# Kernel tuning notes

Measured on AMD Instinct MI355X. Metric: run time of the kernel, lower is better.

Reference implementation:

```python
import jax, jax.numpy as jnp
import numpy as np

NBINS = (128, 64, 32)   # knots per stacked transform
N_GENES = 5000
N_ELEM = 4_000_000


def _split_parameters(unnormalized):
    # mirror of QuadraticSplineStack._split_parameters: [heights(n), widths(n-1)] per transform
    splits = []
    for n in NBINS:
        splits += [n, n - 1]
    parts = jnp.split(unnormalized, np.cumsum(splits)[:-1].tolist(), axis=-1)
    return list(zip(parts[0::2], parts[1::2]))


def _bin_search(table, gix, x):
    # vectorized per-element binary search: searchsorted(table[gix], x, side='right') - 1,
    # clamped to valid bin range [0, K-2]. table: [G, K] sorted; gix, x: [N].
    K = table.shape[-1]
    lo = jnp.zeros(x.shape, jnp.int32)
    hi = jnp.full(x.shape, K, jnp.int32)
    for _ in range(int(np.ceil(np.log2(K + 1)))):
        mid = jnp.clip((lo + hi) // 2, 0, K - 1)
        pred = table[gix, mid] <= x
        lo = jnp.where(pred, mid + 1, lo)
        hi = jnp.where(pred, hi, mid)
    return jnp.clip(lo - 1, 0, K - 2)


def _quadratic_spline_forward(x, gix, unnorm_heights, unnorm_widths):
    # per-gene tables
    widths = jax.nn.softmax(unnorm_widths, axis=-1)                      # [G, n-1]
    locs = jnp.cumsum(widths, axis=-1)
    locs = jnp.pad(locs.at[:, -1].set(1.0), ((0, 0), (1, 0)))            # [G, n] bin_locations
    eh = jnp.exp(unnorm_heights)                                         # [G, n]
    area = jnp.sum(0.5 * (eh[:, :-1] + eh[:, 1:]) * widths, axis=-1, keepdims=True)
    heights = eh / area                                                  # pdf knot heights, integrates to 1
    cdf = jnp.cumsum(0.5 * (heights[:, :-1] + heights[:, 1:]) * widths, axis=-1)
    left_cdf = jnp.pad(cdf.at[:, -1].set(1.0), ((0, 0), (1, 0)))         # [G, n] bin_left_cdf

    # locate bin per element, then gather scalar coefficients
    b = _bin_search(locs, gix, x)                                        # [N] in [0, n-2]
    w = widths[gix, b]
    lh = heights[gix, b]
    rh = heights[gix, b + 1]
    bl = locs[gix, b]
    lc = left_cdf[gix, b]

    alpha = (x - bl) / w
    out = (0.5 * (rh - lh) * w) * alpha * alpha + (lh * w) * alpha + lc
    out = jnp.clip(out, 0.0, 1.0)
    logabsdet = jnp.log(alpha * (rh - lh) + lh)
    return out, logabsdet


def setup_inputs() -> dict:
    key = jax.random.key(0)
    k1, k2, k3 = jax.random.split(key, 3)
    x = jax.random.uniform(k1, (N_ELEM,), dtype=jnp.float32, minval=1e-4, maxval=1.0 - 1e-4)
    local_gene_ix = jax.random.randint(k2, (N_ELEM,), 0, N_GENES)
    total = sum(n + (n - 1) for n in NBINS)  # 445
    unnormalized = jax.random.normal(k3, (N_GENES, total), dtype=jnp.float32) * 0.1
    return {"x": x, "local_gene_ix": local_gene_ix, "unnormalized": unnormalized}


def reference(x, local_gene_ix, unnormalized):
    gix = local_gene_ix.astype(jnp.int32)
    outputs = x
    logabsdet = jnp.zeros_like(x)
    for uh, uw in _split_parameters(unnormalized):
        outputs, lad = _quadratic_spline_forward(outputs, gix, uh, uw)
        logabsdet = logabsdet + lad
    return outputs, logabsdet
```

## Files before the change

### kernel.cpp

```cpp
#include <hip/hip_runtime.h>
#include <hip/hip_bf16.h>
#include <hip/hip_fp16.h>

#define N_GENES_MAX 5000
#define PARAMS_PER_GENE 445

#define KNOTS_PER_GENE 224

__device__ uint2 g_knots[(size_t)N_GENES_MAX * KNOTS_PER_GENE];

static __device__ __forceinline__ unsigned short f2h(float f) {
    union { __half h; unsigned short u; } c;
    c.h = __float2half_rn(f);
    return c.u;
}
static __device__ __forceinline__ float h2f(unsigned short u) {
    union { unsigned short u; __half h; } c;
    c.u = u;
    return __half2float(c.h);
}

__global__ void build_knots(const float* __restrict__ params) {
    const int g = blockIdx.x;
    const int t = blockIdx.y;
    const int ns[3]   = {128, 64, 32};
    const int poff[3] = {0, 255, 382};
    const int koff[3] = {0, 128, 192};

    const int n = ns[t];
    const int m = n - 1;
    const float* ph = params + (size_t)g * PARAMS_PER_GENE + poff[t];
    const float* pw = ph + n;

    __shared__ float s_scan[128];
    __shared__ float s_h[129];
    __shared__ float s_red[128];
    __shared__ float s_loc[128];
    __shared__ float s_cdf[128];

    const int tid = threadIdx.x;

    float uw = (tid < m) ? pw[tid] : -1e30f;
    s_red[tid] = uw;
    __syncthreads();
    for (int s = 64; s > 0; s >>= 1) {
        if (tid < s) s_red[tid] = fmaxf(s_red[tid], s_red[tid + s]);
        __syncthreads();
    }
    const float mx = s_red[0];
    __syncthreads();
    float e = (tid < m) ? expf(uw - mx) : 0.0f;

    s_scan[tid] = e;
    __syncthreads();
    #pragma unroll
    for (int off = 1; off < 128; off <<= 1) {
        float v = (tid >= off) ? s_scan[tid - off] : 0.0f;
        __syncthreads();
        s_scan[tid] += v;
        __syncthreads();
    }
    const float S = s_scan[m - 1];
    const float invS = 1.0f / S;
    const float w_i = e * invS;
    if (tid == 0) s_loc[0] = 0.0f;
    if (tid < m) s_loc[tid + 1] = (tid == m - 1) ? 1.0f : s_scan[tid] * invS;
    __syncthreads();

    float uh = (tid < n) ? ph[tid] : 0.0f;
    float eh = (tid < n) ? expf(uh) : 0.0f;
    s_h[tid] = eh;
    if (tid == 0) s_h[128] = 0.0f;
    __syncthreads();
    float term = (tid < m) ? 0.5f * (s_h[tid] + s_h[tid + 1]) * w_i : 0.0f;
    s_red[tid] = term;
    __syncthreads();
    for (int s = 64; s > 0; s >>= 1) {
        if (tid < s) s_red[tid] += s_red[tid + s];
        __syncthreads();
    }
    const float area = s_red[0];
    __syncthreads();
    const float inv_area = 1.0f / area;
    const float hgt = eh * inv_area;

    float d = term * inv_area;
    s_scan[tid] = d;
    __syncthreads();
    #pragma unroll
    for (int off = 1; off < 128; off <<= 1) {
        float v = (tid >= off) ? s_scan[tid - off] : 0.0f;
        __syncthreads();
        s_scan[tid] += v;
        __syncthreads();
    }
    if (tid == 0) s_cdf[0] = 0.0f;
    if (tid < m) s_cdf[tid + 1] = (tid == m - 1) ? 1.0f : s_scan[tid];
    __syncthreads();

    if (tid < n) {
        uint2 kt;
        kt.x = __float_as_uint(s_loc[tid]);
        kt.y = ((unsigned)f2h(s_cdf[tid]) << 16) | (unsigned)f2h(hgt);
        g_knots[(size_t)g * KNOTS_PER_GENE + koff[t] + tid] = kt;
    }
}

template <int K>
__device__ __forceinline__ void spline_stage(const uint2* __restrict__ kn,
                                             float& x, float& lad) {
    int b = (int)(x * (float)(K - 1));
    b = (b < 0) ? 0 : ((b > K - 2) ? K - 2 : b);
    uint2 k0 = kn[b];
    uint2 k1 = kn[b + 1];
    float l0 = __uint_as_float(k0.x);
    float l1 = __uint_as_float(k1.x);
    while (b > 0 && l0 > x) {
        --b;
        k1 = k0; l1 = l0;
        k0 = kn[b]; l0 = __uint_as_float(k0.x);
    }
    while (b < K - 2 && l1 <= x) {
        ++b;
        k0 = k1; l0 = l1;
        k1 = kn[b + 1]; l1 = __uint_as_float(k1.x);
    }
    const float lh = h2f((unsigned short)(k0.y & 0xffffu));
    const float lc = h2f((unsigned short)(k0.y >> 16));
    const float rh = h2f((unsigned short)(k1.y & 0xffffu));
    const float w  = l1 - l0;
    const float alpha = (x - l0) / w;
    float o = (0.5f * (rh - lh) * w) * alpha * alpha + (lh * w) * alpha + lc;
    o = fminf(fmaxf(o, 0.0f), 1.0f);
    lad += __logf(alpha * (rh - lh) + lh);
    x = o;
}

__global__ void spline_eval_gather(const float* __restrict__ x_in,
                                   const int* __restrict__ gix,
                                   float* __restrict__ out, int N) {
    const int i = blockIdx.x * blockDim.x + threadIdx.x;
    if (i >= N) return;
    float x = x_in[i];
    const uint2* tab = g_knots + (size_t)gix[i] * KNOTS_PER_GENE;
    float lad = 0.0f;
    spline_stage<128>(tab, x, lad);
    spline_stage<64>(tab + 128, x, lad);
    spline_stage<32>(tab + 192, x, lad);
    out[i] = x;
    out[N + i] = lad;
}

extern "C" void kernel_launch(void* const* d_in, const int* in_sizes, int n_in,
                              void* d_out, int out_size, void* d_ws, size_t ws_size,
                              hipStream_t stream) {
    const float* x      = (const float*)d_in[0];
    const int*   gix    = (const int*)d_in[1];
    const float* params = (const float*)d_in[2];
    float* out = (float*)d_out;

    const int N = in_sizes[0];
    const int G = in_sizes[2] / PARAMS_PER_GENE;

    build_knots<<<dim3(G, 3), 128, 0, stream>>>(params);

    const int block = 256;
    spline_eval_gather<<<(N + block - 1) / block, block, 0, stream>>>(x, gix, out, N);
}
```

Baseline: 212.2 us.

## Split knot tables per stage, use wave shuffles, process two elements per thread

The knot table is split into three separate per-stage arrays instead of one interleaved array per gene. The table-building kernel replaces its shared-memory tree reductions and scans with 64-lane wave shuffle primitives and fast exp. The stored CDF is now an fp16 offset relative to the knot location, which aims to reduce quantization error. The eval kernel handles two elements per thread using vectorized nontemporal loads and stores, which raises per-thread work and exposes more independent gathers at the cost of fewer threads.

```diff
diff --git a/kernel.cpp b/kernel.cpp
--- a/kernel.cpp
+++ b/kernel.cpp
@@ -5,19 +5,39 @@
 #define N_GENES_MAX 5000
 #define PARAMS_PER_GENE 445
 
-#define KNOTS_PER_GENE 224
-
-__device__ uint2 g_knots[(size_t)N_GENES_MAX * KNOTS_PER_GENE];
-
-static __device__ __forceinline__ unsigned short f2h(float f) {
+__device__ uint2 g_k0[(size_t)N_GENES_MAX * 128];
+__device__ uint2 g_k1[(size_t)N_GENES_MAX * 64];
+__device__ uint2 g_k2[(size_t)N_GENES_MAX * 32];
+
+static __device__ __forceinline__ unsigned f2h(float f) {
     union { __half h; unsigned short u; } c;
     c.h = __float2half_rn(f);
-    return c.u;
-}
-static __device__ __forceinline__ float h2f(unsigned short u) {
+    return (unsigned)c.u;
+}
+static __device__ __forceinline__ float h2f(unsigned u) {
     union { unsigned short u; __half h; } c;
-    c.u = u;
+    c.u = (unsigned short)u;
     return __half2float(c.h);
+}
+
+static __device__ __forceinline__ float wscan_incl(float v) {
+    const int lane = threadIdx.x & 63;
+    #pragma unroll
+    for (int off = 1; off < 64; off <<= 1) {
+        float u = __shfl_up(v, off, 64);
+        if (lane >= off) v += u;
+    }
+    return v;
+}
+static __device__ __forceinline__ float wmax64(float v) {
+    #pragma unroll
+    for (int off = 32; off > 0; off >>= 1) v = fmaxf(v, __shfl_xor(v, off, 64));
+    return v;
+}
+static __device__ __forceinline__ float wsum64(float v) {
+    #pragma unroll
+    for (int off = 32; off > 0; off >>= 1) v += __shfl_xor(v, off, 64);
+    return v;
 }
 
 __global__ void build_knots(const float* __restrict__ params) {
@@ -25,89 +45,83 @@
     const int t = blockIdx.y;
     const int ns[3]   = {128, 64, 32};
     const int poff[3] = {0, 255, 382};
-    const int koff[3] = {0, 128, 192};
 
     const int n = ns[t];
     const int m = n - 1;
     const float* ph = params + (size_t)g * PARAMS_PER_GENE + poff[t];
     const float* pw = ph + n;
 
+    __shared__ float s2[2];
     __shared__ float s_scan[128];
     __shared__ float s_h[129];
-    __shared__ float s_red[128];
     __shared__ float s_loc[128];
     __shared__ float s_cdf[128];
 
-    const int tid = threadIdx.x;
-
-    float uw = (tid < m) ? pw[tid] : -1e30f;
-    s_red[tid] = uw;
-    __syncthreads();
-    for (int s = 64; s > 0; s >>= 1) {
-        if (tid < s) s_red[tid] = fmaxf(s_red[tid], s_red[tid + s]);
-        __syncthreads();
-    }
-    const float mx = s_red[0];
-    __syncthreads();
-    float e = (tid < m) ? expf(uw - mx) : 0.0f;
-
-    s_scan[tid] = e;
-    __syncthreads();
-    #pragma unroll
-    for (int off = 1; off < 128; off <<= 1) {
-        float v = (tid >= off) ? s_scan[tid - off] : 0.0f;
-        __syncthreads();
-        s_scan[tid] += v;
-        __syncthreads();
-    }
+    const int tid  = threadIdx.x;
+    const int lane = tid & 63;
+    const int wv   = tid >> 6;
+
+    const float uw = (tid < m) ? pw[tid] : -1e30f;
+    float vmax = wmax64(uw);
+    if (lane == 0) s2[wv] = vmax;
+    __syncthreads();
+    const float mx = fmaxf(s2[0], s2[1]);
+    __syncthreads();
+
+    const float e = (tid < m) ? __expf(uw - mx) : 0.0f;
+
+    float sc = wscan_incl(e);
+    if (lane == 63) s2[wv] = sc;
+    __syncthreads();
+    if (wv == 1) sc += s2[0];
+    s_scan[tid] = sc;
+    __syncthreads();
+
     const float S = s_scan[m - 1];
     const float invS = 1.0f / S;
-    const float w_i = e * invS;
     if (tid == 0) s_loc[0] = 0.0f;
     if (tid < m) s_loc[tid + 1] = (tid == m - 1) ? 1.0f : s_scan[tid] * invS;
-    __syncthreads();
-
-    float uh = (tid < n) ? ph[tid] : 0.0f;
-    float eh = (tid < n) ? expf(uh) : 0.0f;
+    const float w_i = e * invS;
+
+    const float eh = (tid < n) ? __expf(ph[tid]) : 0.0f;
     s_h[tid] = eh;
     if (tid == 0) s_h[128] = 0.0f;
     __syncthreads();
-    float term = (tid < m) ? 0.5f * (s_h[tid] + s_h[tid + 1]) * w_i : 0.0f;
-    s_red[tid] = term;
-    __syncthreads();
-    for (int s = 64; s > 0; s >>= 1) {
-        if (tid < s) s_red[tid] += s_red[tid + s];
-        __syncthreads();
-    }
-    const float area = s_red[0];
-    __syncthreads();
-    const float inv_area = 1.0f / area;
-    const float hgt = eh * inv_area;
-
-    float d = term * inv_area;
-    s_scan[tid] = d;
-    __syncthreads();
-    #pragma unroll
-    for (int off = 1; off < 128; off <<= 1) {
-        float v = (tid >= off) ? s_scan[tid - off] : 0.0f;
-        __syncthreads();
-        s_scan[tid] += v;
-        __syncthreads();
-    }
+
+    const float term = (tid < m) ? 0.5f * (s_h[tid] + s_h[tid + 1]) * w_i : 0.0f;
+    float ts = wsum64(term);
+    if (lane == 0) s2[wv] = ts;
+    __syncthreads();
+    const float area = s2[0] + s2[1];
+    __syncthreads();
+
+    const float ia = 1.0f / area;
+    const float hgt = eh * ia;
+
+    float c = wscan_incl(term * ia);
+    if (lane == 63) s2[wv] = c;
+    __syncthreads();
+    if (wv == 1) c += s2[0];
+    s_scan[tid] = c;
+    __syncthreads();
+
     if (tid == 0) s_cdf[0] = 0.0f;
     if (tid < m) s_cdf[tid + 1] = (tid == m - 1) ? 1.0f : s_scan[tid];
     __syncthreads();
 
     if (tid < n) {
+        const float loc = s_loc[tid];
         uint2 kt;
-        kt.x = __float_as_uint(s_loc[tid]);
-        kt.y = ((unsigned)f2h(s_cdf[tid]) << 16) | (unsigned)f2h(hgt);
-        g_knots[(size_t)g * KNOTS_PER_GENE + koff[t] + tid] = kt;
+        kt.x = __float_as_uint(loc);
+        kt.y = (f2h(hgt) << 16) | f2h(s_cdf[tid] - loc);
+        if (t == 0)      g_k0[(size_t)g * 128 + tid] = kt;
+        else if (t == 1) g_k1[(size_t)g * 64 + tid] = kt;
+        else             g_k2[(size_t)g * 32 + tid] = kt;
     }
 }
 
 template <int K>
-__device__ __forceinline__ void spline_stage(const uint2* __restrict__ kn,
+static __device__ __forceinline__ void stage(const uint2* __restrict__ kn,
                                              float& x, float& lad) {
     int b = (int)(x * (float)(K - 1));
     b = (b < 0) ? 0 : ((b > K - 2) ? K - 2 : b);
@@ -125,9 +139,9 @@
         k0 = k1; l0 = l1;
         k1 = kn[b + 1]; l1 = __uint_as_float(k1.x);
     }
-    const float lh = h2f((unsigned short)(k0.y & 0xffffu));
-    const float lc = h2f((unsigned short)(k0.y >> 16));
-    const float rh = h2f((unsigned short)(k1.y & 0xffffu));
+    const float lh = h2f(k0.y >> 16);
+    const float rh = h2f(k1.y >> 16);
+    const float lc = l0 + h2f(k0.y & 0xffffu);
     const float w  = l1 - l0;
     const float alpha = (x - l0) / w;
     float o = (0.5f * (rh - lh) * w) * alpha * alpha + (lh * w) * alpha + lc;
@@ -136,19 +150,38 @@
     x = o;
 }
 
-__global__ void spline_eval_gather(const float* __restrict__ x_in,
-                                   const int* __restrict__ gix,
-                                   float* __restrict__ out, int N) {
+static __device__ __forceinline__ void eval_one(float& x, int g, float& lad) {
+    stage<128>(g_k0 + (size_t)g * 128, x, lad);
+    stage<64> (g_k1 + (size_t)g * 64,  x, lad);
+    stage<32> (g_k2 + (size_t)g * 32,  x, lad);
+}
+
+typedef float fvec2 __attribute__((ext_vector_type(2)));
+typedef int   ivec2 __attribute__((ext_vector_type(2)));
+
+__global__ void spline_eval(const float* __restrict__ x_in,
+                            const int* __restrict__ gix,
+                            float* __restrict__ out, int N) {
     const int i = blockIdx.x * blockDim.x + threadIdx.x;
-    if (i >= N) return;
-    float x = x_in[i];
-    const uint2* tab = g_knots + (size_t)gix[i] * KNOTS_PER_GENE;
-    float lad = 0.0f;
-    spline_stage<128>(tab, x, lad);
-    spline_stage<64>(tab + 128, x, lad);
-    spline_stage<32>(tab + 192, x, lad);
-    out[i] = x;
-    out[N + i] = lad;
+    const int i2 = i * 2;
+    if (i2 + 1 < N) {
+        const fvec2 xv = __builtin_nontemporal_load((const fvec2*)(x_in + i2));
+        const ivec2 gv = __builtin_nontemporal_load((const ivec2*)(gix + i2));
+        float x0 = xv.x, x1 = xv.y;
+        float l0 = 0.0f, l1 = 0.0f;
+        eval_one(x0, gv.x, l0);
+        eval_one(x1, gv.y, l1);
+        fvec2 o0; o0.x = x0; o0.y = x1;
+        fvec2 o1; o1.x = l0; o1.y = l1;
+        __builtin_nontemporal_store(o0, (fvec2*)(out + i2));
+        __builtin_nontemporal_store(o1, (fvec2*)(out + N + i2));
+    } else if (i2 < N) {
+        float x0 = x_in[i2];
+        float l0 = 0.0f;
+        eval_one(x0, gix[i2], l0);
+        out[i2] = x0;
+        out[N + i2] = l0;
+    }
 }
 
 extern "C" void kernel_launch(void* const* d_in, const int* in_sizes, int n_in,
@@ -165,5 +198,6 @@
     build_knots<<<dim3(G, 3), 128, 0, stream>>>(params);
 
     const int block = 256;
-    spline_eval_gather<<<(N + block - 1) / block, block, 0, stream>>>(x, gix, out, N);
-}
+    const int nh = (N + 1) / 2;
+    spline_eval<<<(nh + block - 1) / block, block, 0, stream>>>(x, gix, out, N);
+}
```

Measured after the change: 206.6 us. 1.03x faster.
